# Performance work log

Hardware: AMD Instinct MI355X
Metric: run time of the kernel (lower is better)

## Reference

```python
import jax, jax.numpy as jnp
import numpy as np

B, C, H, W = 4, 256, 64, 64

def setup_inputs() -> dict:
    key = jax.random.key(0)
    ks = jax.random.split(key, 6)
    inv = 1.0 / np.sqrt(C)
    return {
        "feature": jax.random.normal(ks[0], (B, C, H, W), dtype=jnp.float32),
        "flow": jax.random.normal(ks[1], (B, 2, H, W), dtype=jnp.float32),
        "q_w": jax.random.uniform(ks[2], (C, C), dtype=jnp.float32, minval=-inv, maxval=inv),
        "q_b": jax.random.uniform(ks[3], (C,), dtype=jnp.float32, minval=-inv, maxval=inv),
        "k_w": jax.random.uniform(ks[4], (C, C), dtype=jnp.float32, minval=-inv, maxval=inv),
        "k_b": jax.random.uniform(ks[5], (C,), dtype=jnp.float32, minval=-inv, maxval=inv),
    }

def reference(feature, flow, q_w, q_b, k_w, k_b):
    b, c, h, w = feature.shape
    # [b,c,h,w] -> [b, h*w, c] tokens
    tok = feature.reshape(b, c, h * w).transpose(0, 2, 1)
    v = flow.reshape(b, 2, h * w).transpose(0, 2, 1)       # [b, hw, 2]
    q = jnp.einsum('bnc,dc->bnd', tok, q_w) + q_b           # Linear(c,c)
    k = jnp.einsum('bnc,dc->bnd', tok, k_w) + k_b
    scale = 1.0 / jnp.sqrt(jnp.asarray(c, dtype=q.dtype))
    scores = jnp.einsum('bld,bsd->bls', q, k) * scale       # [b, hw, hw]
    attn = jax.nn.softmax(scores, axis=-1)                  # dropout_p=0 -> no-op
    out = jnp.einsum('bls,bsv->blv', attn, v)               # [b, hw, 2]
    return out.reshape(b, h, w, 2).transpose(0, 3, 1, 2)    # [b, 2, h, w]
```

## Files before the change

### kernel.cpp

```cpp
#include <hip/hip_runtime.h>
#include <math.h>

#define BB 4
#define CC 256
#define HWN 4096
#define NTOK 16384
#define SCQ 0.09016844136f

typedef __attribute__((ext_vector_type(8))) short short8;
typedef __attribute__((ext_vector_type(4))) float f32x4;
typedef unsigned short ushort_t;

__device__ __forceinline__ ushort_t f2bf(float f) {
    unsigned int u = __float_as_uint(f);
    unsigned int r = (u + 0x7FFFu + ((u >> 16) & 1u)) >> 16;
    return (ushort_t)r;
}
__device__ __forceinline__ unsigned int pack2(float a, float b) {
    return (unsigned int)f2bf(a) | ((unsigned int)f2bf(b) << 16);
}

__global__ __launch_bounds__(256, 2) void proj_kernel(
    const float* __restrict__ feature,
    const float* __restrict__ q_w, const float* __restrict__ k_w,
    const float* __restrict__ q_bias, const float* __restrict__ k_bias,
    ushort_t* __restrict__ qb, ushort_t* __restrict__ kb,
    float* __restrict__ zbuf)
{
    int gid = blockIdx.x * 256 + threadIdx.x;
    if (gid < 3 * NTOK) zbuf[gid] = 0.f;

    int tt = blockIdx.x & 63;
    int b  = blockIdx.x >> 6;
    int tok0 = tt * 64;

    int t = threadIdx.x, w = t >> 6, lane = t & 63;
    int n16 = lane & 15, quad = lane >> 4;

    __shared__ float    lsA[64][69];
    __shared__ ushort_t lsB[64][264];

    const float* F = feature + (size_t)(b * CC) * HWN;

    int cl = t >> 2, tg = (t & 3) * 16;
    int tokw = t >> 2, c16 = (t & 3) * 16;

    for (int ch = 0; ch < 4; ch++) {
        const float* src = F + (size_t)(ch * 64 + cl) * HWN + tok0 + tg;
        *(float4*)&lsA[cl][tg]      = *(const float4*)(src);
        *(float4*)&lsA[cl][tg + 4]  = *(const float4*)(src + 4);
        *(float4*)&lsA[cl][tg + 8]  = *(const float4*)(src + 8);
        *(float4*)&lsA[cl][tg + 12] = *(const float4*)(src + 12);
        __syncthreads();
        #pragma unroll
        for (int jj = 0; jj < 8; jj++)
            *(unsigned int*)&lsB[tokw][ch * 64 + c16 + 2 * jj] =
                pack2(lsA[c16 + 2 * jj][tokw], lsA[c16 + 2 * jj + 1][tokw]);
        __syncthreads();
    }

    int dw0 = w * 64;
    #pragma unroll
    for (int dsub = 0; dsub < 4; dsub++) {
        int d0 = dw0 + dsub * 16;
        f32x4 accq[4], acck[4];
        #pragma unroll
        for (int i = 0; i < 4; i++) {
            accq[i] = (f32x4){0.f, 0.f, 0.f, 0.f};
            acck[i] = (f32x4){0.f, 0.f, 0.f, 0.f};
        }
        #pragma unroll
        for (int kc = 0; kc < 8; kc++) {
            size_t off = (size_t)(d0 + n16) * CC + kc * 32 + quad * 8;
            float4 a0 = *(const float4*)&q_w[off];
            float4 a1 = *(const float4*)&q_w[off + 4];
            short8 aq, ak;
            aq[0] = (short)f2bf(a0.x * SCQ); aq[1] = (short)f2bf(a0.y * SCQ);
            aq[2] = (short)f2bf(a0.z * SCQ); aq[3] = (short)f2bf(a0.w * SCQ);
            aq[4] = (short)f2bf(a1.x * SCQ); aq[5] = (short)f2bf(a1.y * SCQ);
            aq[6] = (short)f2bf(a1.z * SCQ); aq[7] = (short)f2bf(a1.w * SCQ);
            a0 = *(const float4*)&k_w[off];
            a1 = *(const float4*)&k_w[off + 4];
            ak[0] = (short)f2bf(a0.x); ak[1] = (short)f2bf(a0.y);
            ak[2] = (short)f2bf(a0.z); ak[3] = (short)f2bf(a0.w);
            ak[4] = (short)f2bf(a1.x); ak[5] = (short)f2bf(a1.y);
            ak[6] = (short)f2bf(a1.z); ak[7] = (short)f2bf(a1.w);
            #pragma unroll
            for (int tokt = 0; tokt < 4; tokt++) {
                short8 bf = *(const short8*)&lsB[tokt * 16 + n16][kc * 32 + quad * 8];
                accq[tokt] = __builtin_amdgcn_mfma_f32_16x16x32_bf16(aq, bf, accq[tokt], 0, 0, 0);
                acck[tokt] = __builtin_amdgcn_mfma_f32_16x16x32_bf16(ak, bf, acck[tokt], 0, 0, 0);
            }
        }
        float bqv[4], bkv[4];
        #pragma unroll
        for (int r = 0; r < 4; r++) {
            bqv[r] = q_bias[d0 + quad * 4 + r] * SCQ;
            bkv[r] = k_bias[d0 + quad * 4 + r];
        }
        #pragma unroll
        for (int tokt = 0; tokt < 4; tokt++) {
            size_t row = (size_t)(b * HWN + tok0 + tokt * 16 + n16) * CC + d0 + quad * 4;
            ushort4 oq, ok;
            oq.x = f2bf(accq[tokt][0] + bqv[0]); oq.y = f2bf(accq[tokt][1] + bqv[1]);
            oq.z = f2bf(accq[tokt][2] + bqv[2]); oq.w = f2bf(accq[tokt][3] + bqv[3]);
            ok.x = f2bf(acck[tokt][0] + bkv[0]); ok.y = f2bf(acck[tokt][1] + bkv[1]);
            ok.z = f2bf(acck[tokt][2] + bkv[2]); ok.w = f2bf(acck[tokt][3] + bkv[3]);
            *(ushort4*)&qb[row] = oq;
            *(ushort4*)&kb[row] = ok;
        }
    }
}

__global__ __launch_bounds__(256, 2) void attn_kernel(
    const ushort_t* __restrict__ qb, const ushort_t* __restrict__ kb,
    const float* __restrict__ flow,
    float* __restrict__ den_g, float* __restrict__ nx_g, float* __restrict__ ny_g)
{
    int id = blockIdx.x;
    int qt = id & 15; id >>= 4;
    int sr = id & 7;  id >>= 3;
    int b = id;

    int t = threadIdx.x;
    int w = t >> 6, lane = t & 63;
    int n16 = lane & 15, quad = lane >> 4;

    int q0 = qt * 256 + w * 64;
    int s_beg = sr * 512;

    const ushort_t* Qb = qb + (size_t)b * HWN * CC;
    const ushort_t* Kb = kb + (size_t)b * HWN * CC;

    __shared__ __align__(16) ushort_t lk[2][8192];
    __shared__ float lflow[1024];

    const float* fx = flow + (size_t)b * 2 * HWN;
    const float* fy = fx + HWN;
    lflow[t]        = fx[s_beg + t];
    lflow[t + 256]  = fx[s_beg + t + 256];
    lflow[t + 512]  = fy[s_beg + t];
    lflow[t + 768]  = fy[s_beg + t + 256];

    short8 qf[4][8];
    #pragma unroll
    for (int tq = 0; tq < 4; tq++)
        #pragma unroll
        for (int c = 0; c < 8; c++)
            qf[tq][c] = *(const short8*)&Qb[(size_t)(q0 + tq * 16 + n16) * CC
                                            + c * 32 + quad * 8];

    int srcoff[4];
    #pragma unroll
    for (int i = 0; i < 4; i++) {
        int G = i * 256 + t;
        int r = G >> 5, j = G & 31;
        srcoff[i] = (r * 32 + (j ^ r)) * 16;
    }
    int p16[8];
    #pragma unroll
    for (int c = 0; c < 8; c++)
        p16[c] = (((c * 4 + quad) ^ n16) & 31) * 16;

    float den[4][4], nxa[4][4], nya[4][4];
    #pragma unroll
    for (int tq = 0; tq < 4; tq++)
        #pragma unroll
        for (int r = 0; r < 4; r++) { den[tq][r] = 0.f; nxa[tq][r] = 0.f; nya[tq][r] = 0.f; }

    {
        const char* gsrc = (const char*)(Kb + (size_t)s_beg * CC);
        char* ldst = (char*)lk[0] + t * 16;
        #pragma unroll
        for (int i = 0; i < 4; i++)
            __builtin_amdgcn_global_load_lds(
                (const __attribute__((address_space(1))) unsigned int*)(gsrc + srcoff[i]),
                (__attribute__((address_space(3))) unsigned int*)(ldst + i * 4096),
                16, 0, 0);
    }

    for (int st = 0; st < 16; st++) {
        __syncthreads();
        if (st + 1 < 16) {
            const char* gsrc = (const char*)(Kb + (size_t)(s_beg + (st + 1) * 32) * CC);
            char* ldst = (char*)lk[(st + 1) & 1] + t * 16;
            #pragma unroll
            for (int i = 0; i < 4; i++)
                __builtin_amdgcn_global_load_lds(
                    (const __attribute__((address_space(1))) unsigned int*)(gsrc + srcoff[i]),
                    (__attribute__((address_space(3))) unsigned int*)(ldst + i * 4096),
                    16, 0, 0);
        }
        const char* base = (const char*)lk[st & 1];

        #pragma unroll
        for (int bt = 0; bt < 2; bt++) {
            int rbase = (bt * 16 + n16) * 512;
            int x16   = bt ? 256 : 0;
            f32x4 a0 = {0.f, 0.f, 0.f, 0.f};
            f32x4 a1 = {0.f, 0.f, 0.f, 0.f};
            f32x4 a2 = {0.f, 0.f, 0.f, 0.f};
            f32x4 a3 = {0.f, 0.f, 0.f, 0.f};
            #pragma unroll
            for (int c = 0; c < 8; c++) {
                short8 kf = *(const short8*)(base + rbase + (p16[c] ^ x16));
                a0 = __builtin_amdgcn_mfma_f32_16x16x32_bf16(qf[0][c], kf, a0, 0, 0, 0);
                a1 = __builtin_amdgcn_mfma_f32_16x16x32_bf16(qf[1][c], kf, a1, 0, 0, 0);
                a2 = __builtin_amdgcn_mfma_f32_16x16x32_bf16(qf[2][c], kf, a2, 0, 0, 0);
                a3 = __builtin_amdgcn_mfma_f32_16x16x32_bf16(qf[3][c], kf, a3, 0, 0, 0);
            }
            int sidx = st * 32 + bt * 16 + n16;
            float vx = lflow[sidx];
            float vy = lflow[512 + sidx];
            #pragma unroll
            for (int r = 0; r < 4; r++) {
                float p0 = exp2f(a0[r]);
                float p1 = exp2f(a1[r]);
                float p2 = exp2f(a2[r]);
                float p3 = exp2f(a3[r]);
                den[0][r] += p0; den[1][r] += p1; den[2][r] += p2; den[3][r] += p3;
                nxa[0][r] = fmaf(p0, vx, nxa[0][r]); nxa[1][r] = fmaf(p1, vx, nxa[1][r]);
                nxa[2][r] = fmaf(p2, vx, nxa[2][r]); nxa[3][r] = fmaf(p3, vx, nxa[3][r]);
                nya[0][r] = fmaf(p0, vy, nya[0][r]); nya[1][r] = fmaf(p1, vy, nya[1][r]);
                nya[2][r] = fmaf(p2, vy, nya[2][r]); nya[3][r] = fmaf(p3, vy, nya[3][r]);
            }
        }
    }

    #pragma unroll
    for (int tq = 0; tq < 4; tq++)
        #pragma unroll
        for (int r = 0; r < 4; r++) {
            #pragma unroll
            for (int off = 8; off >= 1; off >>= 1) {
                den[tq][r] += __shfl_down(den[tq][r], off, 16);
                nxa[tq][r] += __shfl_down(nxa[tq][r], off, 16);
                nya[tq][r] += __shfl_down(nya[tq][r], off, 16);
            }
        }
    if (n16 == 0) {
        #pragma unroll
        for (int tq = 0; tq < 4; tq++)
            #pragma unroll
            for (int r = 0; r < 4; r++) {
                int qrow = q0 + tq * 16 + quad * 4 + r;
                int gi = b * HWN + qrow;
                atomicAdd(&den_g[gi], den[tq][r]);
                atomicAdd(&nx_g[gi],  nxa[tq][r]);
                atomicAdd(&ny_g[gi],  nya[tq][r]);
            }
    }
}

__global__ __launch_bounds__(256) void finalize_kernel(
    const float* __restrict__ den_g, const float* __restrict__ nx_g,
    const float* __restrict__ ny_g, float* __restrict__ out)
{
    int idx = blockIdx.x * 256 + threadIdx.x;
    int b = idx >> 12, n = idx & 4095;
    float inv = 1.0f / den_g[idx];
    out[(size_t)b * 2 * HWN + n]       = nx_g[idx] * inv;
    out[(size_t)b * 2 * HWN + HWN + n] = ny_g[idx] * inv;
}

extern "C" void kernel_launch(void* const* d_in, const int* in_sizes, int n_in,
                              void* d_out, int out_size, void* d_ws, size_t ws_size,
                              hipStream_t stream) {
    const float* feature = (const float*)d_in[0];
    const float* flow    = (const float*)d_in[1];
    const float* q_w     = (const float*)d_in[2];
    const float* q_b     = (const float*)d_in[3];
    const float* k_w     = (const float*)d_in[4];
    const float* k_b     = (const float*)d_in[5];
    float* out = (float*)d_out;

    ushort_t* qbuf = (ushort_t*)d_ws;
    ushort_t* kbuf = qbuf + (size_t)NTOK * CC;
    float* den = (float*)(kbuf + (size_t)NTOK * CC);
    float* nx  = den + NTOK;
    float* ny  = nx + NTOK;

    proj_kernel<<<256, 256, 0, stream>>>(feature, q_w, k_w, q_b, k_b,
                                         qbuf, kbuf, den);
    attn_kernel<<<512, 256, 0, stream>>>(qbuf, kbuf, flow, den, nx, ny);
    finalize_kernel<<<64, 256, 0, stream>>>(den, nx, ny, out);
}
```

Baseline: 141.2 us.

## Fold Q and K projections into one bilinear matrix applied to features

Rewrites the attention scores algebraically: the product of the Q and K projections becomes a precomputed CC×CC matrix P = Wk^T·Wq (scaled), so only one projection GEMM per token is needed instead of two. Keys become the raw bf16 features, and the key-side bias term is folded into a per-key scalar added before exp2. Terms that depend only on the query row cancel in the softmax and are dropped. The cost is an extra prep kernel to build P and the bias vector, plus rounding the fused matrix to bf16, which can change numerical error.

```diff
diff --git a/kernel.cpp b/kernel.cpp
--- a/kernel.cpp
+++ b/kernel.cpp
@@ -19,102 +19,138 @@
 __device__ __forceinline__ unsigned int pack2(float a, float b) {
     return (unsigned int)f2bf(a) | ((unsigned int)f2bf(b) << 16);
 }
-
-__global__ __launch_bounds__(256, 2) void proj_kernel(
+__device__ __forceinline__ float bf2f(ushort_t u) {
+    return __uint_as_float(((unsigned int)u) << 16);
+}
+
+__global__ __launch_bounds__(256) void prep_kernel(
+    const float* __restrict__ q_w, const float* __restrict__ k_w,
+    const float* __restrict__ q_bias,
+    ushort_t* __restrict__ P, float* __restrict__ w1, float* __restrict__ zbuf)
+{
+    int bid = blockIdx.x, t = threadIdx.x;
+    int gid = bid * 256 + t;
+    if (gid < 3 * NTOK) zbuf[gid] = 0.f;
+
+    int ta = bid & 15, tb = bid >> 4;
+    int a_ = ta * 16 + (t & 15);
+    int b_ = tb * 16 + (t >> 4);
+
+    float acc0 = 0.f, acc1 = 0.f, acc2 = 0.f, acc3 = 0.f;
+    for (int c = 0; c < CC; c += 4) {
+        acc0 = fmaf(k_w[(c + 0) * CC + b_], q_w[(c + 0) * CC + a_], acc0);
+        acc1 = fmaf(k_w[(c + 1) * CC + b_], q_w[(c + 1) * CC + a_], acc1);
+        acc2 = fmaf(k_w[(c + 2) * CC + b_], q_w[(c + 2) * CC + a_], acc2);
+        acc3 = fmaf(k_w[(c + 3) * CC + b_], q_w[(c + 3) * CC + a_], acc3);
+    }
+    P[b_ * CC + a_] = f2bf((acc0 + acc1 + acc2 + acc3) * SCQ);
+
+    if (ta == 0) {
+        int cseg = (t & 15) * 16;
+        float p = 0.f;
+        #pragma unroll
+        for (int cc = 0; cc < 16; cc++)
+            p = fmaf(k_w[(cseg + cc) * CC + b_], q_bias[cseg + cc], p);
+        #pragma unroll
+        for (int off = 8; off >= 1; off >>= 1)
+            p += __shfl_down(p, off, 16);
+        if ((t & 15) == 0) w1[b_] = p * SCQ;
+    }
+}
+
+__global__ __launch_bounds__(256, 2) void tproj_kernel(
     const float* __restrict__ feature,
-    const float* __restrict__ q_w, const float* __restrict__ k_w,
-    const float* __restrict__ q_bias, const float* __restrict__ k_bias,
-    ushort_t* __restrict__ qb, ushort_t* __restrict__ kb,
-    float* __restrict__ zbuf)
+    const ushort_t* __restrict__ P, const float* __restrict__ w1,
+    ushort_t* __restrict__ fq, ushort_t* __restrict__ ft,
+    float* __restrict__ tv)
 {
-    int gid = blockIdx.x * 256 + threadIdx.x;
-    if (gid < 3 * NTOK) zbuf[gid] = 0.f;
-
-    int tt = blockIdx.x & 63;
-    int b  = blockIdx.x >> 6;
-    int tok0 = tt * 64;
+    int tt = blockIdx.x & 127;
+    int b  = blockIdx.x >> 7;
+    int tok0 = tt * 32;
 
     int t = threadIdx.x, w = t >> 6, lane = t & 63;
     int n16 = lane & 15, quad = lane >> 4;
 
-    __shared__ float    lsA[64][69];
-    __shared__ ushort_t lsB[64][264];
+    __shared__ float    lsA[64][34];
+    __shared__ ushort_t lsB[32][264];
 
     const float* F = feature + (size_t)(b * CC) * HWN;
 
-    int cl = t >> 2, tg = (t & 3) * 16;
-    int tokw = t >> 2, c16 = (t & 3) * 16;
+    int cl = t >> 2, tg = (t & 3) * 8;
+    int tokw = t >> 3, c8 = (t & 7) * 8;
 
     for (int ch = 0; ch < 4; ch++) {
         const float* src = F + (size_t)(ch * 64 + cl) * HWN + tok0 + tg;
-        *(float4*)&lsA[cl][tg]      = *(const float4*)(src);
-        *(float4*)&lsA[cl][tg + 4]  = *(const float4*)(src + 4);
-        *(float4*)&lsA[cl][tg + 8]  = *(const float4*)(src + 8);
-        *(float4*)&lsA[cl][tg + 12] = *(const float4*)(src + 12);
+        float4 v0 = *(const float4*)src;
+        float4 v1 = *(const float4*)(src + 4);
+        *(float2*)&lsA[cl][tg]     = make_float2(v0.x, v0.y);
+        *(float2*)&lsA[cl][tg + 2] = make_float2(v0.z, v0.w);
+        *(float2*)&lsA[cl][tg + 4] = make_float2(v1.x, v1.y);
+        *(float2*)&lsA[cl][tg + 6] = make_float2(v1.z, v1.w);
         __syncthreads();
-        #pragma unroll
-        for (int jj = 0; jj < 8; jj++)
-            *(unsigned int*)&lsB[tokw][ch * 64 + c16 + 2 * jj] =
-                pack2(lsA[c16 + 2 * jj][tokw], lsA[c16 + 2 * jj + 1][tokw]);
+        uint4 o;
+        o.x = pack2(lsA[c8 + 0][tokw], lsA[c8 + 1][tokw]);
+        o.y = pack2(lsA[c8 + 2][tokw], lsA[c8 + 3][tokw]);
+        o.z = pack2(lsA[c8 + 4][tokw], lsA[c8 + 5][tokw]);
+        o.w = pack2(lsA[c8 + 6][tokw], lsA[c8 + 7][tokw]);
+        *(uint4*)&lsB[tokw][ch * 64 + c8] = o;
+        *(uint4*)&ft[(size_t)(b * HWN + tok0 + tokw) * CC + ch * 64 + c8] = o;
         __syncthreads();
     }
 
+    {
+        int tok = t >> 3, cs = (t & 7) * 32;
+        float tp = 0.f;
+        #pragma unroll
+        for (int cc = 0; cc < 32; cc++)
+            tp = fmaf(bf2f(lsB[tok][cs + cc]), w1[cs + cc], tp);
+        #pragma unroll
+        for (int off = 4; off >= 1; off >>= 1)
+            tp += __shfl_xor(tp, off, 8);
+        if ((t & 7) == 0) tv[b * HWN + tok0 + tok] = tp;
+    }
+
     int dw0 = w * 64;
+    short8 ap[8], ap2[8];
+    #pragma unroll
+    for (int kc = 0; kc < 8; kc++)
+        ap[kc] = *(const short8*)&P[(size_t)(dw0 + n16) * CC + kc * 32 + quad * 8];
+
     #pragma unroll
     for (int dsub = 0; dsub < 4; dsub++) {
         int d0 = dw0 + dsub * 16;
-        f32x4 accq[4], acck[4];
-        #pragma unroll
-        for (int i = 0; i < 4; i++) {
-            accq[i] = (f32x4){0.f, 0.f, 0.f, 0.f};
-            acck[i] = (f32x4){0.f, 0.f, 0.f, 0.f};
-        }
+        if (dsub < 3) {
+            #pragma unroll
+            for (int kc = 0; kc < 8; kc++)
+                ap2[kc] = *(const short8*)&P[(size_t)(d0 + 16 + n16) * CC + kc * 32 + quad * 8];
+        }
+        f32x4 acc[2];
+        acc[0] = (f32x4){0.f, 0.f, 0.f, 0.f};
+        acc[1] = (f32x4){0.f, 0.f, 0.f, 0.f};
         #pragma unroll
         for (int kc = 0; kc < 8; kc++) {
-            size_t off = (size_t)(d0 + n16) * CC + kc * 32 + quad * 8;
-            float4 a0 = *(const float4*)&q_w[off];
-            float4 a1 = *(const float4*)&q_w[off + 4];
-            short8 aq, ak;
-            aq[0] = (short)f2bf(a0.x * SCQ); aq[1] = (short)f2bf(a0.y * SCQ);
-            aq[2] = (short)f2bf(a0.z * SCQ); aq[3] = (short)f2bf(a0.w * SCQ);
-            aq[4] = (short)f2bf(a1.x * SCQ); aq[5] = (short)f2bf(a1.y * SCQ);
-            aq[6] = (short)f2bf(a1.z * SCQ); aq[7] = (short)f2bf(a1.w * SCQ);
-            a0 = *(const float4*)&k_w[off];
-            a1 = *(const float4*)&k_w[off + 4];
-            ak[0] = (short)f2bf(a0.x); ak[1] = (short)f2bf(a0.y);
-            ak[2] = (short)f2bf(a0.z); ak[3] = (short)f2bf(a0.w);
-            ak[4] = (short)f2bf(a1.x); ak[5] = (short)f2bf(a1.y);
-            ak[6] = (short)f2bf(a1.z); ak[7] = (short)f2bf(a1.w);
-            #pragma unroll
-            for (int tokt = 0; tokt < 4; tokt++) {
+            #pragma unroll
+            for (int tokt = 0; tokt < 2; tokt++) {
                 short8 bf = *(const short8*)&lsB[tokt * 16 + n16][kc * 32 + quad * 8];
-                accq[tokt] = __builtin_amdgcn_mfma_f32_16x16x32_bf16(aq, bf, accq[tokt], 0, 0, 0);
-                acck[tokt] = __builtin_amdgcn_mfma_f32_16x16x32_bf16(ak, bf, acck[tokt], 0, 0, 0);
-            }
-        }
-        float bqv[4], bkv[4];
-        #pragma unroll
-        for (int r = 0; r < 4; r++) {
-            bqv[r] = q_bias[d0 + quad * 4 + r] * SCQ;
-            bkv[r] = k_bias[d0 + quad * 4 + r];
-        }
-        #pragma unroll
-        for (int tokt = 0; tokt < 4; tokt++) {
+                acc[tokt] = __builtin_amdgcn_mfma_f32_16x16x32_bf16(ap[kc], bf, acc[tokt], 0, 0, 0);
+            }
+        }
+        #pragma unroll
+        for (int tokt = 0; tokt < 2; tokt++) {
             size_t row = (size_t)(b * HWN + tok0 + tokt * 16 + n16) * CC + d0 + quad * 4;
-            ushort4 oq, ok;
-            oq.x = f2bf(accq[tokt][0] + bqv[0]); oq.y = f2bf(accq[tokt][1] + bqv[1]);
-            oq.z = f2bf(accq[tokt][2] + bqv[2]); oq.w = f2bf(accq[tokt][3] + bqv[3]);
-            ok.x = f2bf(acck[tokt][0] + bkv[0]); ok.y = f2bf(acck[tokt][1] + bkv[1]);
-            ok.z = f2bf(acck[tokt][2] + bkv[2]); ok.w = f2bf(acck[tokt][3] + bkv[3]);
-            *(ushort4*)&qb[row] = oq;
-            *(ushort4*)&kb[row] = ok;
-        }
+            ushort4 oq;
+            oq.x = f2bf(acc[tokt][0]); oq.y = f2bf(acc[tokt][1]);
+            oq.z = f2bf(acc[tokt][2]); oq.w = f2bf(acc[tokt][3]);
+            *(ushort4*)&fq[row] = oq;
+        }
+        #pragma unroll
+        for (int kc = 0; kc < 8; kc++) ap[kc] = ap2[kc];
     }
 }
 
 __global__ __launch_bounds__(256, 2) void attn_kernel(
-    const ushort_t* __restrict__ qb, const ushort_t* __restrict__ kb,
-    const float* __restrict__ flow,
+    const ushort_t* __restrict__ fq, const ushort_t* __restrict__ ft,
+    const float* __restrict__ flow, const float* __restrict__ tv,
     float* __restrict__ den_g, float* __restrict__ nx_g, float* __restrict__ ny_g)
 {
     int id = blockIdx.x;
@@ -129,11 +165,11 @@
     int q0 = qt * 256 + w * 64;
     int s_beg = sr * 512;
 
-    const ushort_t* Qb = qb + (size_t)b * HWN * CC;
-    const ushort_t* Kb = kb + (size_t)b * HWN * CC;
+    const ushort_t* Qb = fq + (size_t)b * HWN * CC;
+    const ushort_t* Kb = ft + (size_t)b * HWN * CC;
 
     __shared__ __align__(16) ushort_t lk[2][8192];
-    __shared__ float lflow[1024];
+    __shared__ float lflow[1536];
 
     const float* fx = flow + (size_t)b * 2 * HWN;
     const float* fy = fx + HWN;
@@ -141,6 +177,8 @@
     lflow[t + 256]  = fx[s_beg + t + 256];
     lflow[t + 512]  = fy[s_beg + t];
     lflow[t + 768]  = fy[s_beg + t + 256];
+    lflow[t + 1024] = tv[b * HWN + s_beg + t];
+    lflow[t + 1280] = tv[b * HWN + s_beg + t + 256];
 
     short8 qf[4][8];
     #pragma unroll
@@ -210,14 +248,15 @@
                 a3 = __builtin_amdgcn_mfma_f32_16x16x32_bf16(qf[3][c], kf, a3, 0, 0, 0);
             }
             int sidx = st * 32 + bt * 16 + n16;
-            float vx = lflow[sidx];
-            float vy = lflow[512 + sidx];
+            float vx  = lflow[sidx];
+            float vy  = lflow[512 + sidx];
+            float tvv = lflow[1024 + sidx];
             #pragma unroll
             for (int r = 0; r < 4; r++) {
-                float p0 = exp2f(a0[r]);
-                float p1 = exp2f(a1[r]);
-                float p2 = exp2f(a2[r]);
-                float p3 = exp2f(a3[r]);
+                float p0 = exp2f(a0[r] + tvv);
+                float p1 = exp2f(a1[r] + tvv);
+                float p2 = exp2f(a2[r] + tvv);
+                float p3 = exp2f(a3[r] + tvv);
                 den[0][r] += p0; den[1][r] += p1; den[2][r] += p2; den[3][r] += p3;
                 nxa[0][r] = fmaf(p0, vx, nxa[0][r]); nxa[1][r] = fmaf(p1, vx, nxa[1][r]);
                 nxa[2][r] = fmaf(p2, vx, nxa[2][r]); nxa[3][r] = fmaf(p3, vx, nxa[3][r]);
@@ -271,17 +310,19 @@
     const float* q_w     = (const float*)d_in[2];
     const float* q_b     = (const float*)d_in[3];
     const float* k_w     = (const float*)d_in[4];
-    const float* k_b     = (const float*)d_in[5];
     float* out = (float*)d_out;
 
-    ushort_t* qbuf = (ushort_t*)d_ws;
-    ushort_t* kbuf = qbuf + (size_t)NTOK * CC;
-    float* den = (float*)(kbuf + (size_t)NTOK * CC);
+    ushort_t* fq = (ushort_t*)d_ws;
+    ushort_t* ft = fq + (size_t)NTOK * CC;
+    ushort_t* P  = ft + (size_t)NTOK * CC;
+    float* w1  = (float*)(P + (size_t)CC * CC);
+    float* tvb = w1 + CC;
+    float* den = tvb + NTOK;
     float* nx  = den + NTOK;
     float* ny  = nx + NTOK;
 
-    proj_kernel<<<256, 256, 0, stream>>>(feature, q_w, k_w, q_b, k_b,
-                                         qbuf, kbuf, den);
-    attn_kernel<<<512, 256, 0, stream>>>(qbuf, kbuf, flow, den, nx, ny);
+    prep_kernel<<<256, 256, 0, stream>>>(q_w, k_w, q_b, P, w1, den);
+    tproj_kernel<<<512, 256, 0, stream>>>(feature, P, w1, fq, ft, tvb);
+    attn_kernel<<<512, 256, 0, stream>>>(fq, ft, flow, tvb, den, nx, ny);
     finalize_kernel<<<64, 256, 0, stream>>>(den, nx, ny, out);
 }
```

Measured after the change: 163.1 us. 1.16x slower.
